# Optimization experiments

Measured on AMD Instinct MI355X. Metric: run time of the kernel, lower is better.

## Reference

```python
import jax, jax.numpy as jnp
import numpy as np


def _diff_argmax(hm_flat):
    # Mirrors DifferentiableArgmax.forward: 1-based flat argmax as float32.
    return jnp.argmax(hm_flat, axis=-1).astype(jnp.float32) + 1.0


def setup_inputs() -> dict:
    key = jax.random.key(0)
    k1, k2, k3 = jax.random.split(key, 3)
    B, C, H, W = 256, 68, 64, 64
    pred_hm = jax.random.normal(k1, (B, C, H, W), dtype=jnp.float32)
    # face centers somewhere inside a 1024x1024 image
    center = jax.random.uniform(k2, (B, 2), minval=300.0, maxval=700.0, dtype=jnp.float32)
    # typical face_alignment scale (bbox extent / reference_scale)
    scale = jax.random.uniform(k3, (B,), minval=1.5, maxval=3.0, dtype=jnp.float32)
    return {"pred_hm": pred_hm, "center": center, "scale": scale}


def reference(pred_hm, center, scale):
    B, C, H, W = pred_hm.shape
    idx = _diff_argmax(pred_hm.reshape(B, C, H * W))  # [B,C], 1-based
    px = (idx - 1.0) % W + 1.0                        # 1-based column
    py = jnp.floor((idx - 1.0) / H) + 1.0             # 1-based row

    # --- subpixel refine: sign of neighbor differences (non-differentiable in original) ---
    iX = px.astype(jnp.int32) - 1                     # 0-based
    iY = py.astype(jnp.int32) - 1
    iXc = jnp.clip(iX, 1, W - 2)
    iYc = jnp.clip(iY, 1, H - 2)
    b = jnp.arange(B)[:, None]
    c = jnp.arange(C)[None, :]
    dx = pred_hm[b, c, iYc, iXc + 1] - pred_hm[b, c, iYc, iXc - 1]
    dy = pred_hm[b, c, iYc + 1, iXc] - pred_hm[b, c, iYc - 1, iXc]
    interior = (iX > 0) & (iX < W - 1) & (iY > 0) & (iY < H - 1)
    px = px + jnp.where(interior, jnp.sign(dx) * 0.25, 0.0) - 0.5
    py = py + jnp.where(interior, jnp.sign(dy) * 0.25, 0.0) - 0.5

    # --- inverse affine transform (analytic inverse of transform()) ---
    # t = [[res/h,0,res*(-cx/h+.5)],[0,res/h,res*(-cy/h+.5)],[0,0,1]], h=200*scale
    # inv:  x' = x*h/res + cx - 0.5h ;  y' = y*h/res + cy - 0.5h   (res = H)
    h = 200.0 * scale[:, None]                        # [B,1]
    ox = px * (h / H) + center[:, 0:1] - 0.5 * h
    oy = py * (h / H) + center[:, 1:2] - 0.5 * h
    return jnp.stack([ox, oy], axis=-1)               # [B, 68, 2]
```

## Files before the change

kernel.cpp:

```cpp
#include <hip/hip_runtime.h>

#define BB 256
#define CC 68
#define HH 64
#define WW 64

__global__ __launch_bounds__(256) void face_landmark_kernel(
    const float* __restrict__ pred_hm,
    const float* __restrict__ center,
    const float* __restrict__ scale,
    float* __restrict__ out)
{
    const int bc = blockIdx.x;
    const int b  = bc / CC;
    const int tid = threadIdx.x;

    const float* hm = pred_hm + (size_t)bc * (HH * WW);
    const float4* hm4 = (const float4*)hm;

    float best_v = -__builtin_inff();
    int   best_i = 0;
#pragma unroll
    for (int k = 0; k < 4; ++k) {
        const int fi = tid + 256 * k;
        const float4 v = hm4[fi];
        const int base = fi * 4;
        if (v.x > best_v) { best_v = v.x; best_i = base;     }
        if (v.y > best_v) { best_v = v.y; best_i = base + 1; }
        if (v.z > best_v) { best_v = v.z; best_i = base + 2; }
        if (v.w > best_v) { best_v = v.w; best_i = base + 3; }
    }

#pragma unroll
    for (int off = 32; off > 0; off >>= 1) {
        const float ov = __shfl_down(best_v, off, 64);
        const int   oi = __shfl_down(best_i, off, 64);
        if (ov > best_v || (ov == best_v && oi < best_i)) { best_v = ov; best_i = oi; }
    }

    __shared__ float sv[4];
    __shared__ int   si[4];
    const int wave = tid >> 6;
    const int lane = tid & 63;
    if (lane == 0) { sv[wave] = best_v; si[wave] = best_i; }
    __syncthreads();

    if (tid == 0) {
#pragma unroll
        for (int w = 1; w < 4; ++w) {
            if (sv[w] > best_v || (sv[w] == best_v && si[w] < best_i)) {
                best_v = sv[w]; best_i = si[w];
            }
        }

        const int idx = best_i;
        const int iX = idx & (WW - 1);
        const int iY = idx >> 6;
        float px = (float)(iX + 1);
        float py = (float)(iY + 1);

        const bool interior = (iX > 0) && (iX < WW - 1) && (iY > 0) && (iY < HH - 1);
        if (interior) {
            const int iXc = iX < 1 ? 1 : (iX > WW - 2 ? WW - 2 : iX);
            const int iYc = iY < 1 ? 1 : (iY > HH - 2 ? HH - 2 : iY);
            const float dx = hm[iYc * WW + iXc + 1] - hm[iYc * WW + iXc - 1];
            const float dy = hm[(iYc + 1) * WW + iXc] - hm[(iYc - 1) * WW + iXc];
            px += (dx > 0.0f) ? 0.25f : ((dx < 0.0f) ? -0.25f : 0.0f);
            py += (dy > 0.0f) ? 0.25f : ((dy < 0.0f) ? -0.25f : 0.0f);
        }
        px -= 0.5f;
        py -= 0.5f;

        const float h  = 200.0f * scale[b];
        const float hr = h * (1.0f / (float)HH);
        const float ox = px * hr + center[b * 2 + 0] - 0.5f * h;
        const float oy = py * hr + center[b * 2 + 1] - 0.5f * h;

        ((float2*)out)[bc] = make_float2(ox, oy);
    }
}

extern "C" void kernel_launch(void* const* d_in, const int* in_sizes, int n_in,
                              void* d_out, int out_size, void* d_ws, size_t ws_size,
                              hipStream_t stream) {
    const float* pred_hm = (const float*)d_in[0];
    const float* center  = (const float*)d_in[1];
    const float* scale   = (const float*)d_in[2];
    float* out = (float*)d_out;

    face_landmark_kernel<<<dim3(BB * CC), dim3(256), 0, stream>>>(
        pred_hm, center, scale, out);
}
```

Before: 369.4 us.

## Assign one wave per heatmap and drop block-level reduction

Each 64-lane wave now handles a whole 64x64 heatmap, four heatmaps per block, so the shared-memory cross-wave reduction and the block barrier go away. Each lane issues 16 float4 loads instead of 4, which gives more memory-level parallelism per thread. The grid shrinks by a factor of four. Redundant clamping in the refinement step is also removed. The kernel is memory-bound (about 285 MB read), so the benefit depends on whether the barrier and tail overhead were limiting bandwidth.

```diff
diff --git a/kernel.cpp b/kernel.cpp
--- a/kernel.cpp
+++ b/kernel.cpp
@@ -4,6 +4,7 @@
 #define CC 68
 #define HH 64
 #define WW 64
+#define WAVES_PER_BLOCK 4
 
 __global__ __launch_bounds__(256) void face_landmark_kernel(
     const float* __restrict__ pred_hm,
@@ -11,18 +12,19 @@
     const float* __restrict__ scale,
     float* __restrict__ out)
 {
-    const int bc = blockIdx.x;
-    const int b  = bc / CC;
-    const int tid = threadIdx.x;
+    const int wave = threadIdx.x >> 6;
+    const int lane = threadIdx.x & 63;
+    const int bc   = blockIdx.x * WAVES_PER_BLOCK + wave;
+    const int b    = bc / CC;
 
-    const float* hm = pred_hm + (size_t)bc * (HH * WW);
+    const float*  hm  = pred_hm + (size_t)bc * (HH * WW);
     const float4* hm4 = (const float4*)hm;
 
     float best_v = -__builtin_inff();
     int   best_i = 0;
 #pragma unroll
-    for (int k = 0; k < 4; ++k) {
-        const int fi = tid + 256 * k;
+    for (int k = 0; k < 16; ++k) {
+        const int fi = lane + 64 * k;
         const float4 v = hm4[fi];
         const int base = fi * 4;
         if (v.x > best_v) { best_v = v.x; best_i = base;     }
@@ -38,21 +40,7 @@
         if (ov > best_v || (ov == best_v && oi < best_i)) { best_v = ov; best_i = oi; }
     }
 
-    __shared__ float sv[4];
-    __shared__ int   si[4];
-    const int wave = tid >> 6;
-    const int lane = tid & 63;
-    if (lane == 0) { sv[wave] = best_v; si[wave] = best_i; }
-    __syncthreads();
-
-    if (tid == 0) {
-#pragma unroll
-        for (int w = 1; w < 4; ++w) {
-            if (sv[w] > best_v || (sv[w] == best_v && si[w] < best_i)) {
-                best_v = sv[w]; best_i = si[w];
-            }
-        }
-
+    if (lane == 0) {
         const int idx = best_i;
         const int iX = idx & (WW - 1);
         const int iY = idx >> 6;
@@ -61,10 +49,8 @@
 
         const bool interior = (iX > 0) && (iX < WW - 1) && (iY > 0) && (iY < HH - 1);
         if (interior) {
-            const int iXc = iX < 1 ? 1 : (iX > WW - 2 ? WW - 2 : iX);
-            const int iYc = iY < 1 ? 1 : (iY > HH - 2 ? HH - 2 : iY);
-            const float dx = hm[iYc * WW + iXc + 1] - hm[iYc * WW + iXc - 1];
-            const float dy = hm[(iYc + 1) * WW + iXc] - hm[(iYc - 1) * WW + iXc];
+            const float dx = hm[iY * WW + iX + 1] - hm[iY * WW + iX - 1];
+            const float dy = hm[(iY + 1) * WW + iX] - hm[(iY - 1) * WW + iX];
             px += (dx > 0.0f) ? 0.25f : ((dx < 0.0f) ? -0.25f : 0.0f);
             py += (dy > 0.0f) ? 0.25f : ((dy < 0.0f) ? -0.25f : 0.0f);
         }
@@ -88,6 +74,6 @@
     const float* scale   = (const float*)d_in[2];
     float* out = (float*)d_out;
 
-    face_landmark_kernel<<<dim3(BB * CC), dim3(256), 0, stream>>>(
+    face_landmark_kernel<<<dim3((BB * CC) / WAVES_PER_BLOCK), dim3(256), 0, stream>>>(
         pred_hm, center, scale, out);
 }
```

After: 371.6 us. Within noise of the previous version (+0.6%).
